# Kernel optimization log

Measured on AMD Instinct MI355X. Metric: run time of the kernel, lower is better.

## Reference

```python
import jax, jax.numpy as jnp
import numpy as np

B, N = 4096, 2048


def _nrmse(o, t):
    # o, t: [B, 1, N]. Per-sample RMSE over all non-batch elements,
    # normalized by per-sample (max - min) of the target.
    rmse = jnp.sqrt(jnp.mean((o - t) ** 2, axis=(1, 2)))        # [B]
    rng = jnp.max(t, axis=(1, 2)) - jnp.min(t, axis=(1, 2))     # [B]
    return rmse / rng


def setup_inputs() -> dict:
    key = jax.random.key(0)
    ks = jax.random.split(key, 6)
    names = ["o1", "t1", "o2", "t2", "o3", "t3"]
    return {n: jax.random.normal(k, (B, 1, N), dtype=jnp.float32) for n, k in zip(names, ks)}


def reference(o1, t1, o2, t2, o3, t3):
    loss = (0.5 * _nrmse(o1, t1)
            + 0.25 * _nrmse(o2, t2)
            + 0.25 * _nrmse(o3, t3))  # [B]
    return jnp.mean(loss)
```

## Files before the change

### kernel.cpp

```cpp
#include <hip/hip_runtime.h>
#include <math.h>

constexpr int N_ELEM = 2048;
constexpr int BATCH  = 4096;
constexpr int BLOCK  = 256;
constexpr int TASKS  = 3 * BATCH;
constexpr int GRID1  = TASKS / (BLOCK / 64);

__global__ __launch_bounds__(BLOCK)
void wnrmse_stage1(const float* __restrict__ o1, const float* __restrict__ t1,
                   const float* __restrict__ o2, const float* __restrict__ t2,
                   const float* __restrict__ o3, const float* __restrict__ t3,
                   float* __restrict__ partial)
{
    const int tid  = threadIdx.x;
    const int wave = tid >> 6;
    const int lane = tid & 63;
    const int task = blockIdx.x * (BLOCK / 64) + wave;

    const int pair = task >> 12;
    const int row  = task & (BATCH - 1);

    const float* o;
    const float* t;
    float w;
    if (pair == 0)      { o = o1; t = t1; w = 0.50f; }
    else if (pair == 1) { o = o2; t = t2; w = 0.25f; }
    else                { o = o3; t = t3; w = 0.25f; }

    const float4* o4 = (const float4*)(o + (size_t)row * N_ELEM);
    const float4* t4 = (const float4*)(t + (size_t)row * N_ELEM);

    float4 ov[8], tv[8];
#pragma unroll
    for (int j = 0; j < 8; ++j) ov[j] = o4[lane + j * 64];
#pragma unroll
    for (int j = 0; j < 8; ++j) tv[j] = t4[lane + j * 64];

    float s0 = 0.f, s1 = 0.f, s2 = 0.f, s3 = 0.f;
    float tmax = -INFINITY, tmin = INFINITY;
#pragma unroll
    for (int j = 0; j < 8; ++j) {
        float d0 = ov[j].x - tv[j].x;
        float d1 = ov[j].y - tv[j].y;
        float d2 = ov[j].z - tv[j].z;
        float d3 = ov[j].w - tv[j].w;
        s0 += d0 * d0;
        s1 += d1 * d1;
        s2 += d2 * d2;
        s3 += d3 * d3;
        tmax = fmaxf(tmax, fmaxf(fmaxf(tv[j].x, tv[j].y), fmaxf(tv[j].z, tv[j].w)));
        tmin = fminf(tmin, fminf(fminf(tv[j].x, tv[j].y), fminf(tv[j].z, tv[j].w)));
    }
    float ssd = (s0 + s1) + (s2 + s3);

#pragma unroll
    for (int off = 32; off > 0; off >>= 1) {
        ssd  += __shfl_xor(ssd, off, 64);
        tmax  = fmaxf(tmax, __shfl_xor(tmax, off, 64));
        tmin  = fminf(tmin, __shfl_xor(tmin, off, 64));
    }

    __shared__ float s_part[BLOCK / 64];
    if (lane == 0) {
        float rmse = sqrtf(ssd * (1.0f / (float)N_ELEM));
        s_part[wave] = w * rmse / (tmax - tmin);
    }
    __syncthreads();
    if (tid == 0) {
        partial[blockIdx.x] = s_part[0] + s_part[1] + s_part[2] + s_part[3];
    }
}

__global__ __launch_bounds__(BLOCK)
void wnrmse_stage2(const float* __restrict__ partial, float* __restrict__ out)
{
    const int tid = threadIdx.x;
    float s = 0.0f;
    for (int i = tid; i < GRID1; i += BLOCK) s += partial[i];

#pragma unroll
    for (int off = 32; off > 0; off >>= 1) s += __shfl_xor(s, off, 64);

    __shared__ float s_part[BLOCK / 64];
    const int wave = tid >> 6;
    const int lane = tid & 63;
    if (lane == 0) s_part[wave] = s;
    __syncthreads();
    if (tid == 0) {
        float tot = s_part[0] + s_part[1] + s_part[2] + s_part[3];
        out[0] = tot * (1.0f / (float)BATCH);
    }
}

extern "C" void kernel_launch(void* const* d_in, const int* in_sizes, int n_in,
                              void* d_out, int out_size, void* d_ws, size_t ws_size,
                              hipStream_t stream) {
    const float* o1 = (const float*)d_in[0];
    const float* t1 = (const float*)d_in[1];
    const float* o2 = (const float*)d_in[2];
    const float* t2 = (const float*)d_in[3];
    const float* o3 = (const float*)d_in[4];
    const float* t3 = (const float*)d_in[5];
    float* out     = (float*)d_out;
    float* partial = (float*)d_ws;

    wnrmse_stage1<<<GRID1, BLOCK, 0, stream>>>(o1, t1, o2, t2, o3, t3, partial);
    wnrmse_stage2<<<1, BLOCK, 0, stream>>>(partial, out);
}
```

Baseline: 205.7 us.

## Process three rows per wave with double-buffered register prefetch

Shrinks the stage-1 grid to a fixed 1024 blocks, with each wave handling three consecutive rows instead of one. Loads for the next row are issued into a second register buffer before the current row is reduced, and sched_barrier calls keep the compiler from reordering the loads behind the compute. The intent is more memory-level parallelism per wave and fewer blocks to launch and retire. In exchange it roughly doubles register pressure and may give less latency hiding than many resident waves did before.

```diff
diff --git a/kernel.cpp b/kernel.cpp
--- a/kernel.cpp
+++ b/kernel.cpp
@@ -4,10 +4,42 @@
 constexpr int N_ELEM = 2048;
 constexpr int BATCH  = 4096;
 constexpr int BLOCK  = 256;
+constexpr int GRID1  = 1024;
+constexpr int WAVES1 = GRID1 * (BLOCK / 64);
 constexpr int TASKS  = 3 * BATCH;
-constexpr int GRID1  = TASKS / (BLOCK / 64);
+constexpr int RPW    = TASKS / WAVES1;
 
-__global__ __launch_bounds__(BLOCK)
+__device__ __forceinline__ void issue_row(const float4* __restrict__ o4,
+                                          const float4* __restrict__ t4,
+                                          int lane, float4 ov[8], float4 tv[8])
+{
+#pragma unroll
+    for (int j = 0; j < 8; ++j) ov[j] = o4[lane + j * 64];
+#pragma unroll
+    for (int j = 0; j < 8; ++j) tv[j] = t4[lane + j * 64];
+}
+
+__device__ __forceinline__ void consume_row(const float4 ov[8], const float4 tv[8],
+                                            float& ssd, float& tmax, float& tmin)
+{
+    float s0 = 0.f, s1 = 0.f, s2 = 0.f, s3 = 0.f;
+    float mx = -INFINITY, mn = INFINITY;
+#pragma unroll
+    for (int j = 0; j < 8; ++j) {
+        float d0 = ov[j].x - tv[j].x;
+        float d1 = ov[j].y - tv[j].y;
+        float d2 = ov[j].z - tv[j].z;
+        float d3 = ov[j].w - tv[j].w;
+        s0 += d0 * d0;  s1 += d1 * d1;  s2 += d2 * d2;  s3 += d3 * d3;
+        mx = fmaxf(mx, fmaxf(fmaxf(tv[j].x, tv[j].y), fmaxf(tv[j].z, tv[j].w)));
+        mn = fminf(mn, fminf(fminf(tv[j].x, tv[j].y), fminf(tv[j].z, tv[j].w)));
+    }
+    ssd = (s0 + s1) + (s2 + s3);
+    tmax = mx;
+    tmin = mn;
+}
+
+__global__ __launch_bounds__(BLOCK, 1)
 void wnrmse_stage1(const float* __restrict__ o1, const float* __restrict__ t1,
                    const float* __restrict__ o2, const float* __restrict__ t2,
                    const float* __restrict__ o3, const float* __restrict__ t3,
@@ -16,55 +48,60 @@
     const int tid  = threadIdx.x;
     const int wave = tid >> 6;
     const int lane = tid & 63;
-    const int task = blockIdx.x * (BLOCK / 64) + wave;
+    const int gw   = blockIdx.x * (BLOCK / 64) + wave;
+    const int base = gw * RPW;
 
-    const int pair = task >> 12;
-    const int row  = task & (BATCH - 1);
+    const float* const os[3] = { o1, o2, o3 };
+    const float* const ts[3] = { t1, t2, t3 };
+    const float wgt[3] = { 0.50f, 0.25f, 0.25f };
 
-    const float* o;
-    const float* t;
-    float w;
-    if (pair == 0)      { o = o1; t = t1; w = 0.50f; }
-    else if (pair == 1) { o = o2; t = t2; w = 0.25f; }
-    else                { o = o3; t = t3; w = 0.25f; }
+    const float4* o4p[RPW];
+    const float4* t4p[RPW];
+    float wv[RPW];
+#pragma unroll
+    for (int k = 0; k < RPW; ++k) {
+        const int task = base + k;
+        const int pair = task >> 12;
+        const int row  = task & (BATCH - 1);
+        o4p[k] = (const float4*)(os[pair]) + (size_t)row * (N_ELEM / 4);
+        t4p[k] = (const float4*)(ts[pair]) + (size_t)row * (N_ELEM / 4);
+        wv[k]  = wgt[pair];
+    }
 
-    const float4* o4 = (const float4*)(o + (size_t)row * N_ELEM);
-    const float4* t4 = (const float4*)(t + (size_t)row * N_ELEM);
+    float4 A_o[8], A_t[8], B_o[8], B_t[8];
+    float ssd[RPW], tmax[RPW], tmin[RPW];
 
-    float4 ov[8], tv[8];
-#pragma unroll
-    for (int j = 0; j < 8; ++j) ov[j] = o4[lane + j * 64];
-#pragma unroll
-    for (int j = 0; j < 8; ++j) tv[j] = t4[lane + j * 64];
-
-    float s0 = 0.f, s1 = 0.f, s2 = 0.f, s3 = 0.f;
-    float tmax = -INFINITY, tmin = INFINITY;
-#pragma unroll
-    for (int j = 0; j < 8; ++j) {
-        float d0 = ov[j].x - tv[j].x;
-        float d1 = ov[j].y - tv[j].y;
-        float d2 = ov[j].z - tv[j].z;
-        float d3 = ov[j].w - tv[j].w;
-        s0 += d0 * d0;
-        s1 += d1 * d1;
-        s2 += d2 * d2;
-        s3 += d3 * d3;
-        tmax = fmaxf(tmax, fmaxf(fmaxf(tv[j].x, tv[j].y), fmaxf(tv[j].z, tv[j].w)));
-        tmin = fminf(tmin, fminf(fminf(tv[j].x, tv[j].y), fminf(tv[j].z, tv[j].w)));
-    }
-    float ssd = (s0 + s1) + (s2 + s3);
+    issue_row(o4p[0], t4p[0], lane, A_o, A_t);
+    __builtin_amdgcn_sched_barrier(0);
+    issue_row(o4p[1], t4p[1], lane, B_o, B_t);
+    __builtin_amdgcn_sched_barrier(0);
+    consume_row(A_o, A_t, ssd[0], tmax[0], tmin[0]);
+    __builtin_amdgcn_sched_barrier(0);
+    issue_row(o4p[2], t4p[2], lane, A_o, A_t);
+    __builtin_amdgcn_sched_barrier(0);
+    consume_row(B_o, B_t, ssd[1], tmax[1], tmin[1]);
+    __builtin_amdgcn_sched_barrier(0);
+    consume_row(A_o, A_t, ssd[2], tmax[2], tmin[2]);
 
 #pragma unroll
     for (int off = 32; off > 0; off >>= 1) {
-        ssd  += __shfl_xor(ssd, off, 64);
-        tmax  = fmaxf(tmax, __shfl_xor(tmax, off, 64));
-        tmin  = fminf(tmin, __shfl_xor(tmin, off, 64));
+#pragma unroll
+        for (int k = 0; k < RPW; ++k) {
+            ssd[k]  += __shfl_xor(ssd[k], off, 64);
+            tmax[k]  = fmaxf(tmax[k], __shfl_xor(tmax[k], off, 64));
+            tmin[k]  = fminf(tmin[k], __shfl_xor(tmin[k], off, 64));
+        }
     }
 
     __shared__ float s_part[BLOCK / 64];
     if (lane == 0) {
-        float rmse = sqrtf(ssd * (1.0f / (float)N_ELEM));
-        s_part[wave] = w * rmse / (tmax - tmin);
+        float local = 0.f;
+#pragma unroll
+        for (int k = 0; k < RPW; ++k) {
+            float rmse = sqrtf(ssd[k] * (1.0f / (float)N_ELEM));
+            local += wv[k] * rmse / (tmax[k] - tmin[k]);
+        }
+        s_part[wave] = local;
     }
     __syncthreads();
     if (tid == 0) {
```

Result: no change. 205.2 us (-0.2%).
